# Kernel optimization log

Hardware: AMD Instinct MI355X
Metric: run time of the kernel (lower is better)

Reference implementation:

```python
import jax, jax.numpy as jnp
import numpy as np

TEMPERATURE = 0.5
EPS = 1e-12  # torch F.normalize eps


def setup_inputs() -> dict:
    key = jax.random.key(0)
    k1, k2 = jax.random.split(key)
    z_i = jax.random.normal(k1, (32, 128, 128), dtype=jnp.float32)
    z_j = jax.random.normal(k2, (32, 128, 128), dtype=jnp.float32)
    return {"z_i": z_i, "z_j": z_j}


def _l2_normalize(x):
    # matches torch F.normalize(dim=1): x / max(||x||, eps)
    n = jnp.sqrt(jnp.sum(x * x, axis=1, keepdims=True))
    return x / jnp.maximum(n, EPS)


def _off_diagonal(a):
    # rows of a with the diagonal removed, row-major order -> [n, n-1]
    n = a.shape[0]
    return a.reshape(-1)[:-1].reshape(n - 1, n + 1)[:, 1:].reshape(n, n - 1)


def reference(z_i, z_j):
    B, S, D = z_i.shape
    N = B * S
    zi = _l2_normalize(z_i.reshape(N, D))
    zj = _l2_normalize(z_j.reshape(N, D))
    r = jnp.concatenate([zi, zj], axis=0)              # [2N, D]
    sim = r @ r.T                                      # [2N, 2N]
    # positives: off-diagonals at +/-N (unaffected by the diag -inf fill)
    pos = jnp.concatenate([jnp.diagonal(sim, N), jnp.diagonal(sim, -N)])  # [2N]
    # negatives: all non-diagonal entries, row-major (== torch boolean-mask view)
    neg = _off_diagonal(sim)                           # [2N, 2N-1]
    logits = jnp.concatenate([pos[:, None], neg], axis=1) / TEMPERATURE  # [2N, 2N]
    # labels are all 0 -> CE(sum) / 2N == mean of -log_softmax[:, 0]
    loss = -jax.nn.log_softmax(logits, axis=1)[:, 0]
    return jnp.sum(loss) / (2 * N)
```

## Files before the change

kernel.cpp:

```cpp
#include <hip/hip_runtime.h>
#include <hip/hip_bf16.h>
#include <math.h>

#define NPAIR 4096
#define D 128
#define TWO_N 8192
#define NSLAB 32
#define ALPHA 1.6986436f

typedef float f32x4 __attribute__((ext_vector_type(4)));
typedef int i32x8 __attribute__((ext_vector_type(8)));

__device__ __forceinline__ void async_ld16(void* lds, const void* g) {
    __builtin_amdgcn_global_load_lds(
        (__attribute__((address_space(1))) const unsigned int*)g,
        (__attribute__((address_space(3))) unsigned int*)lds, 16, 0, 0);
}

__device__ __forceinline__ i32x8 mk8(uint4 lo, uint4 hi) {
    return (i32x8){(int)lo.x, (int)lo.y, (int)lo.z, (int)lo.w,
                   (int)hi.x, (int)hi.y, (int)hi.z, (int)hi.w};
}

__global__ __launch_bounds__(256) void norm_kernel(const float* __restrict__ zi,
                                                   const float* __restrict__ zj,
                                                   unsigned char* __restrict__ Rb,
                                                   float* __restrict__ pos,
                                                   float* __restrict__ colpart,
                                                   float* __restrict__ out) {
    if (blockIdx.x == 0 && threadIdx.x == 0) out[0] = 0.f;
    if (blockIdx.x < 32) colpart[blockIdx.x * 256 + threadIdx.x] = 0.f;
    int k = blockIdx.x * 8 + (threadIdx.x >> 5);
    int t = threadIdx.x & 31;
    const float4 a = *(const float4*)(zi + k * D + 4 * t);
    const float4 b = *(const float4*)(zj + k * D + 4 * t);
    float si = a.x * a.x + a.y * a.y + a.z * a.z + a.w * a.w;
    float sj = b.x * b.x + b.y * b.y + b.z * b.z + b.w * b.w;
    float dt = a.x * b.x + a.y * b.y + a.z * b.z + a.w * b.w;
    #pragma unroll
    for (int m = 1; m < 32; m <<= 1) {
        si += __shfl_xor(si, m, 32);
        sj += __shfl_xor(sj, m, 32);
        dt += __shfl_xor(dt, m, 32);
    }
    float ii = 1.0f / fmaxf(sqrtf(si), 1e-12f);
    float ij = 1.0f / fmaxf(sqrtf(sj), 1e-12f);
    if (t == 0) pos[k] = dt * ii * ij;
    ii *= ALPHA; ij *= ALPHA;
    int r0 = __builtin_amdgcn_cvt_pk_fp8_f32(a.x * ii, a.y * ii, 0, false);
    r0 = __builtin_amdgcn_cvt_pk_fp8_f32(a.z * ii, a.w * ii, r0, true);
    *(unsigned int*)(Rb + (size_t)k * 128 + 4 * t) = (unsigned int)r0;
    int r1 = __builtin_amdgcn_cvt_pk_fp8_f32(b.x * ij, b.y * ij, 0, false);
    r1 = __builtin_amdgcn_cvt_pk_fp8_f32(b.z * ij, b.w * ij, r1, true);
    *(unsigned int*)(Rb + (size_t)(k + NPAIR) * 128 + 4 * t) = (unsigned int)r1;
}

__global__ __launch_bounds__(256, 4) void simexp_kernel(const unsigned char* __restrict__ Rb,
                                                        float* __restrict__ rspart,
                                                        float* __restrict__ colpart) {
    const int bi = blockIdx.x >> 3;
    const int jc = blockIdx.x & 7;
    const int s = bi >> 4;
    if (jc < s) return;
    const bool emitcol = (jc > s);

    __shared__ uint4 Bs[4][3][128];
    const int tid = threadIdx.x;
    const int wave = tid >> 6, lane = tid & 63;
    const int rp = lane & 15, q = lane >> 4;

    i32x8 afr[4];
    {
        const unsigned char* Ab = Rb + (size_t)(bi * 64 + rp) * 128 + q * 32;
        #pragma unroll
        for (int rt = 0; rt < 4; ++rt) {
            uint4 h0 = *(const uint4*)(Ab + rt * 16 * 128);
            uint4 h1 = *(const uint4*)(Ab + rt * 16 * 128 + 16);
            afr[rt] = mk8(h0, h1);
        }
    }

    const unsigned char* gslab = Rb + (size_t)(jc * 1024 + wave * 16) * 128;
    char* lpanel = (char*)&Bs[wave][0][0];
    const int laneoff = (lane >> 3) * 128 + (((lane & 7) ^ ((lane >> 3) & 7)) << 4);

    float rs[16];
    #pragma unroll
    for (int i = 0; i < 16; ++i) rs[i] = 0.f;

    #pragma unroll
    for (int j = 0; j < 2; ++j)
        #pragma unroll
        for (int d = 0; d < 2; ++d)
            async_ld16(lpanel + j * 2048 + d * 1024,
                       gslab + j * 8192 + d * 1024 + laneoff);

    const int diagbase = bi * 64 - jc * 1024;
    const int slot0 = rp * 8;
    const int sw = rp & 7;

    #pragma unroll
    for (int jt = 0; jt < 16; ++jt) {
        if (jt < 14) __builtin_amdgcn_s_waitcnt(0x0F72);
        else         __builtin_amdgcn_s_waitcnt(0x0F70);

        const int cur = jt % 3;
        const uint4* P = &Bs[wave][cur][0];
        uint4 u0 = P[slot0 + ((q * 2 + 0) ^ sw)];
        uint4 u1 = P[slot0 + ((q * 2 + 1) ^ sw)];
        i32x8 bfr = mk8(u0, u1);

        if (jt < 14) {
            const int nb = (jt + 2) % 3;
            #pragma unroll
            for (int d = 0; d < 2; ++d)
                async_ld16(lpanel + nb * 2048 + d * 1024,
                           gslab + (jt + 2) * 8192 + d * 1024 + laneoff);
        }

        f32x4 acc[4] = {};
        #pragma unroll
        for (int rt = 0; rt < 4; ++rt)
            acc[rt] = __builtin_amdgcn_mfma_scale_f32_16x16x128_f8f6f4(
                afr[rt], bfr, acc[rt],
                0, 0,
                0, 0x7F7F7F7F,
                0, 0x7F7F7F7F);

        if (jt * 64 == diagbase) {
            #pragma unroll
            for (int rt = 0; rt < 4; ++rt)
                #pragma unroll
                for (int r = 0; r < 4; ++r) {
                    int ro = rt * 16 + q * 4 + r;
                    int co = wave * 16 + rp;
                    float e = __builtin_amdgcn_exp2f(acc[rt][r]);
                    rs[rt * 4 + r] += (ro == co) ? 0.f : e;
                }
        } else if (emitcol) {
            float csum = 0.f;
            #pragma unroll
            for (int rt = 0; rt < 4; ++rt)
                #pragma unroll
                for (int r = 0; r < 4; ++r) {
                    float e = __builtin_amdgcn_exp2f(acc[rt][r]);
                    rs[rt * 4 + r] += e;
                    csum += e;
                }
            csum += __shfl_xor(csum, 16, 64);
            csum += __shfl_xor(csum, 32, 64);
            if (q == 0)
                atomicAdd(colpart + jc * 1024 + jt * 64 + wave * 16 + rp, csum);
        } else {
            #pragma unroll
            for (int rt = 0; rt < 4; ++rt)
                #pragma unroll
                for (int r = 0; r < 4; ++r)
                    rs[rt * 4 + r] += __builtin_amdgcn_exp2f(acc[rt][r]);
        }
    }

    #pragma unroll
    for (int i = 0; i < 16; ++i) {
        float v = rs[i];
        v += __shfl_xor(v, 1, 64);
        v += __shfl_xor(v, 2, 64);
        v += __shfl_xor(v, 4, 64);
        v += __shfl_xor(v, 8, 64);
        rs[i] = v;
    }
    if (rp == 0) {
        const int slab = jc * 4 + wave;
        const int rowb = bi * 64 + q * 4;
        #pragma unroll
        for (int rt = 0; rt < 4; ++rt)
            #pragma unroll
            for (int r = 0; r < 4; ++r)
                rspart[(size_t)(rowb + rt * 16 + r) * NSLAB + slab] = rs[rt * 4 + r];
    }
}

__global__ __launch_bounds__(128) void finalize_kernel(const float* __restrict__ rspart,
                                                       const float* __restrict__ colpart,
                                                       const float* __restrict__ pos,
                                                       float* __restrict__ out) {
    __shared__ float red[2];
    int tid = threadIdx.x;
    int k = blockIdx.x * 128 + tid;
    int s = k >> 10;
    const f32x4* v = (const f32x4*)(rspart + (size_t)k * NSLAB);
    f32x4 sv = {0.f, 0.f, 0.f, 0.f};
    for (int p4 = s; p4 < 8; ++p4) sv += v[p4];
    float rsum = sv.x + sv.y + sv.z + sv.w + colpart[k];
    float ps = pos[k & (NPAIR - 1)];
    float p2 = ps + ps;
    float local = logf(rsum + __expf(p2)) - p2;
    #pragma unroll
    for (int m = 1; m < 64; m <<= 1) local += __shfl_xor(local, m, 64);
    if ((tid & 63) == 0) red[tid >> 6] = local;
    __syncthreads();
    if (tid == 0) atomicAdd(out, (red[0] + red[1]) * (1.0f / (float)TWO_N));
}

extern "C" void kernel_launch(void* const* d_in, const int* in_sizes, int n_in,
                              void* d_out, int out_size, void* d_ws, size_t ws_size,
                              hipStream_t stream) {
    const float* zi = (const float*)d_in[0];
    const float* zj = (const float*)d_in[1];
    char* ws = (char*)d_ws;
    unsigned char* Rb = (unsigned char*)ws;
    float* rspart = (float*)(ws + 1 * 1024 * 1024);
    float* pos = (float*)(ws + 2 * 1024 * 1024);
    float* colpart = (float*)(ws + 2 * 1024 * 1024 + 16 * 1024);

    norm_kernel<<<NPAIR / 8, 256, 0, stream>>>(zi, zj, Rb, pos, colpart, (float*)d_out);
    simexp_kernel<<<128 * 8, 256, 0, stream>>>(Rb, rspart, colpart);
    finalize_kernel<<<64, 128, 0, stream>>>(rspart, colpart, pos, (float*)d_out);
}
```

Baseline: 81.73 us.

## Balance symmetric sim tiles across blocks with a flattened upper-triangle schedule

Before, the grid was 128 row blocks by 8 column chunks, and blocks below the diagonal exited early, which left work unevenly spread. Now the 8256 upper-triangular 64x64 tiles are split evenly across 1024 blocks. Each block decodes its starting (row, column) tile with a sqrt formula and walks tiles in row-major order, crossing row boundaries and reloading A fragments as it goes. Row sums are now accumulated with atomics into a single rowsum array instead of per-slab partials, so finalize becomes simpler. The cost is a runtime loop bound (less unrolling), extra atomics on row changes, and more branching inside the loop.

```diff
diff --git a/kernel.cpp b/kernel.cpp
--- a/kernel.cpp
+++ b/kernel.cpp
@@ -5,7 +5,7 @@
 #define NPAIR 4096
 #define D 128
 #define TWO_N 8192
-#define NSLAB 32
+#define NTILES 8256
 #define ALPHA 1.6986436f
 
 typedef float f32x4 __attribute__((ext_vector_type(4)));
@@ -26,10 +26,12 @@
                                                    const float* __restrict__ zj,
                                                    unsigned char* __restrict__ Rb,
                                                    float* __restrict__ pos,
+                                                   float* __restrict__ rowsum,
                                                    float* __restrict__ colpart,
                                                    float* __restrict__ out) {
     if (blockIdx.x == 0 && threadIdx.x == 0) out[0] = 0.f;
-    if (blockIdx.x < 32) colpart[blockIdx.x * 256 + threadIdx.x] = 0.f;
+    if (blockIdx.x < 32)       colpart[blockIdx.x * 256 + threadIdx.x] = 0.f;
+    else if (blockIdx.x < 64)  rowsum[(blockIdx.x - 32) * 256 + threadIdx.x] = 0.f;
     int k = blockIdx.x * 8 + (threadIdx.x >> 5);
     int t = threadIdx.x & 31;
     const float4 a = *(const float4*)(zi + k * D + 4 * t);
@@ -56,18 +58,28 @@
 }
 
 __global__ __launch_bounds__(256, 4) void simexp_kernel(const unsigned char* __restrict__ Rb,
-                                                        float* __restrict__ rspart,
+                                                        float* __restrict__ rowsum,
                                                         float* __restrict__ colpart) {
-    const int bi = blockIdx.x >> 3;
-    const int jc = blockIdx.x & 7;
-    const int s = bi >> 4;
-    if (jc < s) return;
-    const bool emitcol = (jc > s);
-
-    __shared__ uint4 Bs[4][3][128];
     const int tid = threadIdx.x;
     const int wave = tid >> 6, lane = tid & 63;
     const int rp = lane & 15, q = lane >> 4;
+
+    const int b = blockIdx.x;
+    const int g0 = (NTILES * b) >> 10;
+    const int g1 = (NTILES * (b + 1)) >> 10;
+    const int nt = g1 - g0;
+
+    int bi = (int)((257.0f - sqrtf(66049.0f - 8.0f * (float)g0)) * 0.5f);
+    if (bi < 0) bi = 0; if (bi > 127) bi = 127;
+    while (bi * (257 - bi) / 2 > g0) --bi;
+    while ((bi + 1) * (256 - bi) / 2 <= g0) ++bi;
+    int j64 = bi + (g0 - bi * (257 - bi) / 2);
+
+    __shared__ uint4 Bs[4][3][128];
+    char* lpanel = (char*)&Bs[wave][0][0];
+    const int laneoff = (lane >> 3) * 128 + (((lane & 7) ^ ((lane >> 3) & 7)) << 4);
+    const int slot0 = rp * 8;
+    const int sw = rp & 7;
 
     i32x8 afr[4];
     {
@@ -79,55 +91,76 @@
             afr[rt] = mk8(h0, h1);
         }
     }
-
-    const unsigned char* gslab = Rb + (size_t)(jc * 1024 + wave * 16) * 128;
-    char* lpanel = (char*)&Bs[wave][0][0];
-    const int laneoff = (lane >> 3) * 128 + (((lane & 7) ^ ((lane >> 3) & 7)) << 4);
-
     float rs[16];
     #pragma unroll
     for (int i = 0; i < 16; ++i) rs[i] = 0.f;
-
-    #pragma unroll
-    for (int j = 0; j < 2; ++j)
-        #pragma unroll
-        for (int d = 0; d < 2; ++d)
-            async_ld16(lpanel + j * 2048 + d * 1024,
-                       gslab + j * 8192 + d * 1024 + laneoff);
-
-    const int diagbase = bi * 64 - jc * 1024;
-    const int slot0 = rp * 8;
-    const int sw = rp & 7;
-
-    #pragma unroll
-    for (int jt = 0; jt < 16; ++jt) {
-        if (jt < 14) __builtin_amdgcn_s_waitcnt(0x0F72);
-        else         __builtin_amdgcn_s_waitcnt(0x0F70);
-
-        const int cur = jt % 3;
-        const uint4* P = &Bs[wave][cur][0];
+    int aBi = bi;
+
+    int wBi = bi, wJ = j64;
+    #pragma unroll
+    for (int j = 0; j < 2; ++j) {
+        if (j < nt) {
+            const unsigned char* gp = Rb + (size_t)(wJ * 64 + wave * 16) * 128 + laneoff;
+            async_ld16(lpanel + j * 2048, gp);
+            async_ld16(lpanel + j * 2048 + 1024, gp + 1024);
+            if (++wJ == 128) { ++wBi; wJ = wBi; }
+        }
+    }
+
+    int cBi = bi, cJ = j64;
+    int cur = 0;
+
+    for (int i = 0; i < nt; ++i) {
+        if (cBi != aBi) {
+            #pragma unroll
+            for (int t2 = 0; t2 < 16; ++t2) {
+                float v = rs[t2];
+                v += __shfl_xor(v, 1, 64);
+                v += __shfl_xor(v, 2, 64);
+                v += __shfl_xor(v, 4, 64);
+                v += __shfl_xor(v, 8, 64);
+                if (rp == 0)
+                    atomicAdd(rowsum + aBi * 64 + (t2 >> 2) * 16 + q * 4 + (t2 & 3), v);
+                rs[t2] = 0.f;
+            }
+            const unsigned char* Ab = Rb + (size_t)(cBi * 64 + rp) * 128 + q * 32;
+            #pragma unroll
+            for (int rt = 0; rt < 4; ++rt) {
+                uint4 h0 = *(const uint4*)(Ab + rt * 16 * 128);
+                uint4 h1 = *(const uint4*)(Ab + rt * 16 * 128 + 16);
+                afr[rt] = mk8(h0, h1);
+            }
+            aBi = cBi;
+        }
+
+        if (i < nt - 2) __builtin_amdgcn_s_waitcnt(0x0F72);
+        else            __builtin_amdgcn_s_waitcnt(0x0F70);
+
+        const uint4* P = &Bs[wave][0][0] + cur * 128;
         uint4 u0 = P[slot0 + ((q * 2 + 0) ^ sw)];
         uint4 u1 = P[slot0 + ((q * 2 + 1) ^ sw)];
         i32x8 bfr = mk8(u0, u1);
 
-        if (jt < 14) {
-            const int nb = (jt + 2) % 3;
-            #pragma unroll
-            for (int d = 0; d < 2; ++d)
-                async_ld16(lpanel + nb * 2048 + d * 1024,
-                           gslab + (jt + 2) * 8192 + d * 1024 + laneoff);
-        }
-
-        f32x4 acc[4] = {};
+        if (i + 2 < nt) {
+            const int nb = (cur >= 1) ? cur - 1 : 2;
+            const unsigned char* gp = Rb + (size_t)(wJ * 64 + wave * 16) * 128 + laneoff;
+            async_ld16(lpanel + nb * 2048, gp);
+            async_ld16(lpanel + nb * 2048 + 1024, gp + 1024);
+            if (++wJ == 128) { ++wBi; wJ = wBi; }
+        }
+
+        f32x4 acc[4];
         #pragma unroll
-        for (int rt = 0; rt < 4; ++rt)
+        for (int rt = 0; rt < 4; ++rt) {
+            f32x4 z = {0.f, 0.f, 0.f, 0.f};
             acc[rt] = __builtin_amdgcn_mfma_scale_f32_16x16x128_f8f6f4(
-                afr[rt], bfr, acc[rt],
+                afr[rt], bfr, z,
                 0, 0,
                 0, 0x7F7F7F7F,
                 0, 0x7F7F7F7F);
-
-        if (jt * 64 == diagbase) {
+        }
+
+        if (cJ == cBi) {
             #pragma unroll
             for (int rt = 0; rt < 4; ++rt)
                 #pragma unroll
@@ -137,7 +170,7 @@
                     float e = __builtin_amdgcn_exp2f(acc[rt][r]);
                     rs[rt * 4 + r] += (ro == co) ? 0.f : e;
                 }
-        } else if (emitcol) {
+        } else {
             float csum = 0.f;
             #pragma unroll
             for (int rt = 0; rt < 4; ++rt)
@@ -150,48 +183,33 @@
             csum += __shfl_xor(csum, 16, 64);
             csum += __shfl_xor(csum, 32, 64);
             if (q == 0)
-                atomicAdd(colpart + jc * 1024 + jt * 64 + wave * 16 + rp, csum);
-        } else {
-            #pragma unroll
-            for (int rt = 0; rt < 4; ++rt)
-                #pragma unroll
-                for (int r = 0; r < 4; ++r)
-                    rs[rt * 4 + r] += __builtin_amdgcn_exp2f(acc[rt][r]);
-        }
-    }
-
-    #pragma unroll
-    for (int i = 0; i < 16; ++i) {
-        float v = rs[i];
+                atomicAdd(colpart + cJ * 64 + wave * 16 + rp, csum);
+        }
+
+        cur = (cur == 2) ? 0 : cur + 1;
+        if (++cJ == 128) { ++cBi; cJ = cBi; }
+    }
+
+    #pragma unroll
+    for (int t2 = 0; t2 < 16; ++t2) {
+        float v = rs[t2];
         v += __shfl_xor(v, 1, 64);
         v += __shfl_xor(v, 2, 64);
         v += __shfl_xor(v, 4, 64);
         v += __shfl_xor(v, 8, 64);
-        rs[i] = v;
-    }
-    if (rp == 0) {
-        const int slab = jc * 4 + wave;
-        const int rowb = bi * 64 + q * 4;
-        #pragma unroll
-        for (int rt = 0; rt < 4; ++rt)
-            #pragma unroll
-            for (int r = 0; r < 4; ++r)
-                rspart[(size_t)(rowb + rt * 16 + r) * NSLAB + slab] = rs[rt * 4 + r];
-    }
-}
-
-__global__ __launch_bounds__(128) void finalize_kernel(const float* __restrict__ rspart,
+        if (rp == 0)
+            atomicAdd(rowsum + aBi * 64 + (t2 >> 2) * 16 + q * 4 + (t2 & 3), v);
+    }
+}
+
+__global__ __launch_bounds__(128) void finalize_kernel(const float* __restrict__ rowsum,
                                                        const float* __restrict__ colpart,
                                                        const float* __restrict__ pos,
                                                        float* __restrict__ out) {
     __shared__ float red[2];
     int tid = threadIdx.x;
     int k = blockIdx.x * 128 + tid;
-    int s = k >> 10;
-    const f32x4* v = (const f32x4*)(rspart + (size_t)k * NSLAB);
-    f32x4 sv = {0.f, 0.f, 0.f, 0.f};
-    for (int p4 = s; p4 < 8; ++p4) sv += v[p4];
-    float rsum = sv.x + sv.y + sv.z + sv.w + colpart[k];
+    float rsum = rowsum[k] + colpart[k];
     float ps = pos[k & (NPAIR - 1)];
     float p2 = ps + ps;
     float local = logf(rsum + __expf(p2)) - p2;
@@ -209,11 +227,11 @@
     const float* zj = (const float*)d_in[1];
     char* ws = (char*)d_ws;
     unsigned char* Rb = (unsigned char*)ws;
-    float* rspart = (float*)(ws + 1 * 1024 * 1024);
-    float* pos = (float*)(ws + 2 * 1024 * 1024);
-    float* colpart = (float*)(ws + 2 * 1024 * 1024 + 16 * 1024);
-
-    norm_kernel<<<NPAIR / 8, 256, 0, stream>>>(zi, zj, Rb, pos, colpart, (float*)d_out);
-    simexp_kernel<<<128 * 8, 256, 0, stream>>>(Rb, rspart, colpart);
-    finalize_kernel<<<64, 128, 0, stream>>>(rspart, colpart, pos, (float*)d_out);
-}
+    float* rowsum = (float*)(ws + 1 * 1024 * 1024);
+    float* colpart = (float*)(ws + 1 * 1024 * 1024 + 32 * 1024);
+    float* pos = (float*)(ws + 1 * 1024 * 1024 + 64 * 1024);
+
+    norm_kernel<<<NPAIR / 8, 256, 0, stream>>>(zi, zj, Rb, pos, rowsum, colpart, (float*)d_out);
+    simexp_kernel<<<1024, 256, 0, stream>>>(Rb, rowsum, colpart);
+    finalize_kernel<<<64, 128, 0, stream>>>(rowsum, colpart, pos, (float*)d_out);
+}
```

After: 86.99 us. +6.4%, slower.
